# Performance work log

Hardware: AMD Instinct MI355X
Metric: run time of the kernel (lower is better)

The kernel has to match this reference:

```python
import jax, jax.numpy as jnp
import numpy as np

N = 50000
SELF_LOOP_W = 2.0  # GCNConv(improved=True)


def gcn_conv(x, edge_index, W, b):
    # x: [N, Fin], edge_index: [2, E] (row=source, col=target)
    h = x @ W  # [N, Fout]
    row, col = edge_index[0], edge_index[1]
    ones = jnp.ones(row.shape[0], dtype=h.dtype)
    deg = jax.ops.segment_sum(ones, col, num_segments=N) + SELF_LOOP_W
    dinv = jnp.where(deg > 0, jax.lax.rsqrt(deg), 0.0)
    norm = dinv[row] * dinv[col]  # [E]
    agg = jax.ops.segment_sum(norm[:, None] * h[row], col, num_segments=N)
    # self-loop contribution: weight 2.0, norm = dinv[i]^2
    agg = agg + (SELF_LOOP_W * dinv * dinv)[:, None] * h
    return agg + b


def setup_inputs() -> dict:
    key = jax.random.key(0)
    ks = jax.random.split(key, 12)
    F_in, H1, H2, H3 = 256, 256, 128, 64
    E, Ep, En = 800000, 200000, 200000
    def glorot(k, shape):
        lim = np.sqrt(6.0 / (shape[0] + shape[1]))
        return jax.random.uniform(k, shape, jnp.float32, -lim, lim)
    return {
        "x": jax.random.normal(ks[0], (N, F_in), jnp.float32),
        "train_edge_index": jax.random.randint(ks[1], (2, E), 0, N),
        "pos_edge_index": jax.random.randint(ks[2], (2, Ep), 0, N),
        "neg_edge_index": jax.random.randint(ks[3], (2, En), 0, N),
        "W1": glorot(ks[4], (F_in, H1)),
        "b1": jnp.zeros((H1,), jnp.float32),
        "W2": glorot(ks[5], (H1, H2)),
        "b2": jnp.zeros((H2,), jnp.float32),
        "Wl1": glorot(ks[6], (H2, H3)),
        "bl1": jnp.zeros((H3,), jnp.float32),
        "Wl2": glorot(ks[7], (H3, 1)),
        "bl2": jnp.zeros((1,), jnp.float32),
    }


def reference(x, train_edge_index, pos_edge_index, neg_edge_index,
              W1, b1, W2, b2, Wl1, bl1, Wl2, bl2):
    h = jax.nn.relu(gcn_conv(x, train_edge_index, W1, b1))
    h = gcn_conv(h, train_edge_index, W2, b2)  # [N, 128]
    tei = jnp.concatenate([pos_edge_index, neg_edge_index], axis=-1)  # [2, Ep+En]
    e = h[tei[1]] + h[tei[0]]  # x_i + x_j, [Etot, 128]
    e = jax.nn.relu(e @ Wl1 + bl1)
    e = jax.nn.sigmoid(e @ Wl2 + bl2)
    return e.reshape(-1)
```

## Files before the change

kernel.cpp:

```cpp
#include <hip/hip_runtime.h>
#include <math.h>

#define NV 50000
#define ETR 800000
#define EPOS 200000
#define ETEST 400000

typedef __attribute__((ext_vector_type(8))) short bf16x8;
typedef __attribute__((ext_vector_type(8))) unsigned short ushortx8;
typedef __attribute__((ext_vector_type(4))) float f32x4;

__device__ inline unsigned short f2b(float f) {
    union { float f; unsigned u; } v; v.f = f;
    unsigned r = v.u + 0x7fffu + ((v.u >> 16) & 1u);
    return (unsigned short)(r >> 16);
}
__device__ inline float blo(unsigned q) { union { unsigned u; float f; } v; v.u = q << 16; return v.f; }
__device__ inline float bhi(unsigned q) { union { unsigned u; float f; } v; v.u = q & 0xffff0000u; return v.f; }
__device__ inline float b2f(unsigned short s) { union { unsigned u; float f; } v; v.u = ((unsigned)s) << 16; return v.f; }

__device__ inline ushortx8 bf16add8(ushortx8 a, ushortx8 b) {
    ushortx8 r;
    #pragma unroll
    for (int i = 0; i < 8; ++i)
        r[i] = f2b(b2f(a[i]) + b2f(b[i]));
    return r;
}

#define GLOAD_LDS16(g, l) __builtin_amdgcn_global_load_lds( \
    (__attribute__((address_space(1))) void*)(g), \
    (__attribute__((address_space(3))) void*)(l), 16, 0, 0)


template<int N, int K, bool AF32>
__device__ __forceinline__ void gemm_body(
    const void* __restrict__ Av, const unsigned short* __restrict__ Bt,
    unsigned short* __restrict__ C, int M, int row0, int col0)
{
    constexpr int BK = 64;
    __shared__ unsigned short smem[18464];
    unsigned short (*Asm)[BK] = (unsigned short (*)[BK])smem;
    unsigned short (*Bsm)[BK] = (unsigned short (*)[BK])(smem + 8192);
    int tid = threadIdx.x;
    int lane = tid & 63, wid = tid >> 6;
    int wr = wid >> 1, wc = wid & 1;

    int sr = tid >> 3;
    int s8 = tid & 7;
    int fr = lane & 15;
    int g  = lane >> 4;

    f32x4 acc[4][4] = {};

    for (int k0 = 0; k0 < K; k0 += BK) {
        #pragma unroll
        for (int i = 0; i < 4; ++i) {
            int r = sr + i * 32;
            int gr = row0 + r;
            int s8sw = s8 ^ (r & 7);
            GLOAD_LDS16(&Bt[(size_t)(col0 + r) * K + k0 + s8sw * 8], &Bsm[r][s8 * 8]);
            if constexpr (AF32) {
                const float* Af = (const float*)Av;
                ushortx8 va = {0, 0, 0, 0, 0, 0, 0, 0};
                if (gr < M) {
                    float4 f0 = *(const float4*)&Af[(size_t)gr * K + k0 + s8 * 8];
                    float4 f1 = *(const float4*)&Af[(size_t)gr * K + k0 + s8 * 8 + 4];
                    va[0] = f2b(f0.x); va[1] = f2b(f0.y); va[2] = f2b(f0.z); va[3] = f2b(f0.w);
                    va[4] = f2b(f1.x); va[5] = f2b(f1.y); va[6] = f2b(f1.z); va[7] = f2b(f1.w);
                }
                *(ushortx8*)&Asm[r][(s8 ^ (r & 7)) * 8] = va;
            } else {
                const unsigned short* Ab = (const unsigned short*)Av;
                GLOAD_LDS16(&Ab[(size_t)gr * K + k0 + s8sw * 8], &Asm[r][s8 * 8]);
            }
        }
        __syncthreads();
        #pragma unroll
        for (int kf = 0; kf < BK; kf += 32) {
            int sbase = kf >> 3;
            bf16x8 af[4], bfr[4];
            #pragma unroll
            for (int m = 0; m < 4; ++m) {
                int rr = wr * 64 + m * 16 + fr;
                af[m] = *(const bf16x8*)&Asm[rr][((sbase + g) ^ (fr & 7)) * 8];
            }
            #pragma unroll
            for (int n = 0; n < 4; ++n) {
                int rr = wc * 64 + n * 16 + fr;
                bfr[n] = *(const bf16x8*)&Bsm[rr][((sbase + g) ^ (fr & 7)) * 8];
            }
            #pragma unroll
            for (int m = 0; m < 4; ++m)
                #pragma unroll
                for (int n = 0; n < 4; ++n)
                    acc[m][n] = __builtin_amdgcn_mfma_f32_16x16x32_bf16(af[m], bfr[n], acc[m][n], 0, 0, 0);
        }
        __syncthreads();
    }

    {
        unsigned short* cw = smem + wid * 4616;
        #pragma unroll
        for (int m = 0; m < 4; ++m)
            #pragma unroll
            for (int n = 0; n < 4; ++n)
                #pragma unroll
                for (int j = 0; j < 4; ++j)
                    cw[(m * 16 + g * 4 + j) * 72 + n * 16 + fr] = f2b(acc[m][n][j]);
        __syncthreads();
        int row = tid >> 1;
        int half = tid & 1;
        int q = ((row >> 6) << 1) + half;
        int rl = row & 63;
        const unsigned short* cr = smem + q * 4616 + rl * 72;
        int gr = row0 + row;
        if (gr < M) {
            unsigned short* gp = C + (size_t)gr * N + col0 + half * 64;
            #pragma unroll
            for (int c8 = 0; c8 < 8; ++c8)
                *(ushortx8*)&gp[c8 * 8] = *(const ushortx8*)&cr[c8 * 8];
        }
    }
}


__global__ __launch_bounds__(256) void fat0_kernel(
    const int* __restrict__ tei, int* __restrict__ deg,
    const float* __restrict__ W1, unsigned short* __restrict__ w1t)
{
    int bid = blockIdx.x;
    int t = threadIdx.x;
    if (bid < 3125) {
        int e = bid * 256 + t;
        if (e < ETR) atomicAdd(&deg[tei[ETR + e]], 1);
    } else {
        int i = (bid - 3125) * 256 + t;
        w1t[i] = f2b(W1[(i & 255) * 256 + (i >> 8)]);
    }
}


__global__ __launch_bounds__(1024) void ptr2_kernel(
    const int* __restrict__ deg, int* __restrict__ ptr,
    int* __restrict__ cursor, float* __restrict__ dinv)
{
    int b = blockIdx.x, t = threadIdx.x;
    int lane = t & 63, w = t >> 6;
    __shared__ int wred[16], wsum[16], woff[16];
    __shared__ int base_s;

    int pre = 0;
    int lim = b * 1024;
    for (int i = t; i < lim; i += 1024) pre += deg[i];
    #pragma unroll
    for (int off = 32; off > 0; off >>= 1) pre += __shfl_xor(pre, off);
    if (lane == 0) wred[w] = pre;
    __syncthreads();
    if (t == 0) {
        int s = 0;
        #pragma unroll
        for (int k = 0; k < 16; ++k) s += wred[k];
        base_s = s;
    }

    int i = b * 1024 + t;
    int d = (i < NV) ? deg[i] : 0;
    int v = d;
    #pragma unroll
    for (int off = 1; off < 64; off <<= 1) {
        int u = __shfl_up(v, off);
        if (lane >= off) v += u;
    }
    if (lane == 63) wsum[w] = v;
    __syncthreads();
    if (t == 0) {
        int s = base_s;
        #pragma unroll
        for (int k = 0; k < 16; ++k) { woff[k] = s; s += wsum[k]; }
    }
    __syncthreads();
    int excl = woff[w] + v - d;
    if (i < NV) {
        ptr[i] = excl;
        cursor[i] = excl;
        dinv[i] = rsqrtf((float)d + 2.0f);
        if (i == NV - 1) ptr[NV] = excl + d;
    }
}


__global__ __launch_bounds__(256) void fat1_kernel(
    const float* __restrict__ x, const unsigned short* __restrict__ w1t,
    unsigned short* __restrict__ h1lin,
    const int* __restrict__ tei, const float* __restrict__ dinv,
    int* __restrict__ cursor, int2* __restrict__ edat,
    const float* __restrict__ W2, unsigned short* __restrict__ w2t,
    const float* __restrict__ Wl1, unsigned short* __restrict__ wl1t)
{
    int bid = blockIdx.x;
    int t = threadIdx.x;
    if (bid < 782) {
        int row0 = (bid >> 1) * 128, col0 = (bid & 1) * 128;
        gemm_body<256, 256, true>(x, w1t, h1lin, NV, row0, col0);
    } else if (bid < 3907) {
        int e = (bid - 782) * 256 + t;
        if (e < ETR) {
            int row = tei[e];
            int col = tei[ETR + e];
            int p = atomicAdd(&cursor[col], 1);
            edat[p] = make_int2(row, __float_as_int(dinv[row] * dinv[col]));
        }
    } else if (bid < 4035) {
        int i = (bid - 3907) * 256 + t;
        w2t[i] = f2b(W2[(i & 255) * 128 + (i >> 8)]);
    } else {
        int i = (bid - 4035) * 256 + t;
        wl1t[i] = f2b(Wl1[(i & 127) * 64 + (i >> 7)]);
    }
}


__global__ __launch_bounds__(256) void gemm2_kernel(
    const unsigned short* __restrict__ A, const unsigned short* __restrict__ Bt,
    unsigned short* __restrict__ C)
{
    gemm_body<128, 256, false>(A, Bt, C, NV, blockIdx.x * 128, 0);
}


template<int F, bool RELU>
__global__ __launch_bounds__(256) void gather_kernel(
    const int* __restrict__ ptr, const int2* __restrict__ edat,
    const float* __restrict__ dinv, const unsigned short* __restrict__ hlin,
    const float* __restrict__ bias, unsigned short* __restrict__ hout)
{
    constexpr int V = F / 64;
    int gid = blockIdx.x * blockDim.x + threadIdx.x;
    int node = gid >> 6, lane = gid & 63;
    if (node >= NV) return;
    float dc = dinv[node];
    int j0 = ptr[node], j1 = ptr[node + 1];
    float acc[V] = {};
    const unsigned short* hb = hlin + lane * V;
    const long long* edl = (const long long*)edat;

    int j = j0;
    for (; j + 7 < j1; j += 8) {
        long long e[8];
        #pragma unroll
        for (int u = 0; u < 8; ++u) e[u] = __builtin_nontemporal_load(edl + j + u);
        if constexpr (V == 4) {
            uint2 q[8];
            #pragma unroll
            for (int u = 0; u < 8; ++u)
                q[u] = *(const uint2*)(hb + (size_t)(int)e[u] * F);
            #pragma unroll
            for (int u = 0; u < 8; ++u) {
                float n = __int_as_float((int)(e[u] >> 32));
                acc[0] += n * blo(q[u].x);
                acc[1] += n * bhi(q[u].x);
                acc[2] += n * blo(q[u].y);
                acc[3] += n * bhi(q[u].y);
            }
        } else {
            unsigned q[8];
            #pragma unroll
            for (int u = 0; u < 8; ++u)
                q[u] = *(const unsigned*)(hb + (size_t)(int)e[u] * F);
            #pragma unroll
            for (int u = 0; u < 8; ++u) {
                float n = __int_as_float((int)(e[u] >> 32));
                acc[0] += n * blo(q[u]);
                acc[1] += n * bhi(q[u]);
            }
        }
    }
    for (; j + 3 < j1; j += 4) {
        long long e[4];
        #pragma unroll
        for (int u = 0; u < 4; ++u) e[u] = __builtin_nontemporal_load(edl + j + u);
        if constexpr (V == 4) {
            uint2 q[4];
            #pragma unroll
            for (int u = 0; u < 4; ++u)
                q[u] = *(const uint2*)(hb + (size_t)(int)e[u] * F);
            #pragma unroll
            for (int u = 0; u < 4; ++u) {
                float n = __int_as_float((int)(e[u] >> 32));
                acc[0] += n * blo(q[u].x);
                acc[1] += n * bhi(q[u].x);
                acc[2] += n * blo(q[u].y);
                acc[3] += n * bhi(q[u].y);
            }
        } else {
            unsigned q[4];
            #pragma unroll
            for (int u = 0; u < 4; ++u)
                q[u] = *(const unsigned*)(hb + (size_t)(int)e[u] * F);
            #pragma unroll
            for (int u = 0; u < 4; ++u) {
                float n = __int_as_float((int)(e[u] >> 32));
                acc[0] += n * blo(q[u]);
                acc[1] += n * bhi(q[u]);
            }
        }
    }
    for (; j < j1; ++j) {
        long long e0 = __builtin_nontemporal_load(edl + j);
        float n0 = __int_as_float((int)(e0 >> 32));
        if constexpr (V == 4) {
            uint2 q0 = *(const uint2*)(hb + (size_t)(int)e0 * F);
            acc[0] += n0 * blo(q0.x);
            acc[1] += n0 * bhi(q0.x);
            acc[2] += n0 * blo(q0.y);
            acc[3] += n0 * bhi(q0.y);
        } else {
            unsigned q0 = *(const unsigned*)(hb + (size_t)(int)e0 * F);
            acc[0] += n0 * blo(q0);
            acc[1] += n0 * bhi(q0);
        }
    }

    const unsigned short* ps = hb + (size_t)node * F;
    float sw = 2.0f * dc * dc;
    if constexpr (V == 4) {
        uint2 qs = *(const uint2*)ps;
        float o0 = acc[0] + sw * blo(qs.x) + bias[lane * 4 + 0];
        float o1 = acc[1] + sw * bhi(qs.x) + bias[lane * 4 + 1];
        float o2 = acc[2] + sw * blo(qs.y) + bias[lane * 4 + 2];
        float o3 = acc[3] + sw * bhi(qs.y) + bias[lane * 4 + 3];
        if (RELU) {
            o0 = fmaxf(o0, 0.f); o1 = fmaxf(o1, 0.f);
            o2 = fmaxf(o2, 0.f); o3 = fmaxf(o3, 0.f);
        }
        union { unsigned short u[4]; unsigned long long ll; } pk;
        pk.u[0] = f2b(o0); pk.u[1] = f2b(o1); pk.u[2] = f2b(o2); pk.u[3] = f2b(o3);
        __builtin_nontemporal_store(pk.ll, (unsigned long long*)(hout + (size_t)node * F + lane * 4));
    } else {
        unsigned qs = *(const unsigned*)ps;
        float o0 = acc[0] + sw * blo(qs) + bias[lane * 2 + 0];
        float o1 = acc[1] + sw * bhi(qs) + bias[lane * 2 + 1];
        if (RELU) { o0 = fmaxf(o0, 0.f); o1 = fmaxf(o1, 0.f); }
        union { unsigned short u[2]; unsigned q; } pk;
        pk.u[0] = f2b(o0); pk.u[1] = f2b(o1);
        __builtin_nontemporal_store(pk.q, (unsigned*)(hout + (size_t)node * F + lane * 2));
    }
}


__global__ __launch_bounds__(256) void edge_mlp_mfma_kernel(
    const int* __restrict__ pos, const int* __restrict__ neg,
    const unsigned short* __restrict__ h2, const unsigned short* __restrict__ Wl1t,
    const float* __restrict__ bl1, const float* __restrict__ Wl2,
    const float* __restrict__ bl2, float* __restrict__ out)
{
    __shared__ unsigned short Es[128][128];
    __shared__ unsigned short Ws[64][128];
    int tid = threadIdx.x;
    int lane = tid & 63, w = tid >> 6;
    int fr = lane & 15, g = lane >> 4;
    int e0 = blockIdx.x * 128;

    #pragma unroll
    for (int k = 0; k < 4; ++k) {
        int chunk = tid + k * 256;
        int row = chunk >> 4, c = chunk & 15;
        *(ushortx8*)&Ws[row][(c ^ (row & 7)) * 8] = *(const ushortx8*)&Wl1t[chunk * 8];
    }

    int et = tid >> 1, hh = tid & 1;
    int eg = e0 + et;
    int a, b;
    if (eg < EPOS) { a = pos[eg]; b = pos[EPOS + eg]; }
    else { int i = eg - EPOS; a = neg[i]; b = neg[EPOS + i]; }
    const unsigned short* pa = h2 + (size_t)a * 128 + hh * 64;
    const unsigned short* pb = h2 + (size_t)b * 128 + hh * 64;
    #pragma unroll
    for (int c8 = 0; c8 < 8; ++c8) {
        ushortx8 va = *(const ushortx8*)&pa[c8 * 8];
        ushortx8 vb = *(const ushortx8*)&pb[c8 * 8];
        ushortx8 vs = bf16add8(va, vb);
        int c = hh * 8 + c8;
        *(ushortx8*)&Es[et][(c ^ (et & 7)) * 8] = vs;
    }
    __syncthreads();

    f32x4 acc[2][4] = {};
    #pragma unroll
    for (int ks = 0; ks < 4; ++ks) {
        int c = ks * 4 + g;
        bf16x8 af[2], bfr[4];
        #pragma unroll
        for (int m = 0; m < 2; ++m) {
            int r = w * 32 + m * 16 + fr;
            af[m] = *(const bf16x8*)&Es[r][(c ^ (r & 7)) * 8];
        }
        #pragma unroll
        for (int n = 0; n < 4; ++n) {
            int r = n * 16 + fr;
            bfr[n] = *(const bf16x8*)&Ws[r][(c ^ (r & 7)) * 8];
        }
        #pragma unroll
        for (int m = 0; m < 2; ++m)
            #pragma unroll
            for (int n = 0; n < 4; ++n)
                acc[m][n] = __builtin_amdgcn_mfma_f32_16x16x32_bf16(af[m], bfr[n], acc[m][n], 0, 0, 0);
    }

    float bl2v = bl2[0];
    float b1v[4], w2v[4];
    #pragma unroll
    for (int n = 0; n < 4; ++n) {
        b1v[n] = bl1[n * 16 + fr];
        w2v[n] = Wl2[n * 16 + fr];
    }
    #pragma unroll
    for (int m = 0; m < 2; ++m) {
        float p[4];
        #pragma unroll
        for (int j = 0; j < 4; ++j) {
            float s = 0.f;
            #pragma unroll
            for (int n = 0; n < 4; ++n)
                s += fmaxf(acc[m][n][j] + b1v[n], 0.0f) * w2v[n];
            p[j] = s;
        }
        #pragma unroll
        for (int off = 1; off < 16; off <<= 1) {
            #pragma unroll
            for (int j = 0; j < 4; ++j)
                p[j] += __shfl_xor(p[j], off);
        }
        int ebase = e0 + w * 32 + m * 16 + g * 4;
        #pragma unroll
        for (int j = 0; j < 4; ++j)
            if (fr == j)
                out[ebase + j] = 1.0f / (1.0f + expf(-(p[j] + bl2v)));
    }
}


extern "C" void kernel_launch(void* const* d_in, const int* in_sizes, int n_in,
                              void* d_out, int out_size, void* d_ws, size_t ws_size,
                              hipStream_t stream) {
    const float* x   = (const float*)d_in[0];
    const int*   tei = (const int*)d_in[1];
    const int*   pos = (const int*)d_in[2];
    const int*   neg = (const int*)d_in[3];
    const float* W1  = (const float*)d_in[4];
    const float* b1  = (const float*)d_in[5];
    const float* W2  = (const float*)d_in[6];
    const float* b2  = (const float*)d_in[7];
    const float* Wl1 = (const float*)d_in[8];
    const float* bl1 = (const float*)d_in[9];
    const float* Wl2 = (const float*)d_in[10];
    const float* bl2 = (const float*)d_in[11];
    float* out = (float*)d_out;

    float* fws = (float*)d_ws;
    int*   iws = (int*)d_ws;
    unsigned short* usws = (unsigned short*)d_ws;
    float* dinv     = fws;
    int*   deg      = iws + 50000;
    int*   ptr      = iws + 100000;
    int*   cursor   = iws + 150002;
    int2*  edat     = (int2*)(iws + 200064);
    unsigned short* w1t  = usws + 2ull * 1800192;
    unsigned short* w2t  = usws + 2ull * 1832960;
    unsigned short* wl1t = usws + 2ull * 1849344;
    unsigned short* bufX = usws + 2ull * 1853504;
    unsigned short* bufL16 = usws + 2ull * 8253504;
    unsigned short* bufH = usws + 2ull * 14653504;

    hipMemsetAsync(deg, 0, NV * sizeof(int), stream);

    fat0_kernel<<<3381, 256, 0, stream>>>(tei, deg, W1, w1t);

    ptr2_kernel<<<49, 1024, 0, stream>>>(deg, ptr, cursor, dinv);

    fat1_kernel<<<4067, 256, 0, stream>>>(x, w1t, bufL16, tei, dinv, cursor, edat,
                                          W2, w2t, Wl1, wl1t);

    gather_kernel<256, true><<<(NV * 64) / 256, 256, 0, stream>>>(ptr, edat, dinv, bufL16, b1, bufH);

    gemm2_kernel<<<391, 256, 0, stream>>>(bufH, w2t, bufX);
    gather_kernel<128, false><<<(NV * 64) / 256, 256, 0, stream>>>(ptr, edat, dinv, bufX, b2, bufL16);

    edge_mlp_mfma_kernel<<<ETEST / 128, 256, 0, stream>>>(pos, neg, bufL16, wl1t, bl1, Wl2, bl2, out);
}
```

Before: 281.3 us.

## Precompute per-node Wl1 projection then gather-add in edge head

Uses linearity: (h[a]+h[b])@Wl1 = h[a]@Wl1 + h[b]@Wl1, so a node-level GEMM (50k x 128 -> 64, padded to 128 columns with zeroed weights) computes u once, and the edge kernel gathers two 64-wide bf16 rows, adds bias, applies ReLU, dots with Wl2 and applies the sigmoid. This replaces 400k edge-level 128x64 MFMA work and 128-wide gathers with 64-wide gathers plus a smaller node GEMM. The cost is an extra kernel launch, a padded GEMM that wastes half its columns, and bf16 rounding of u before the add, which changes numerics slightly.

```diff
diff --git a/kernel.cpp b/kernel.cpp
--- a/kernel.cpp
+++ b/kernel.cpp
@@ -19,20 +19,12 @@
 __device__ inline float bhi(unsigned q) { union { unsigned u; float f; } v; v.u = q & 0xffff0000u; return v.f; }
 __device__ inline float b2f(unsigned short s) { union { unsigned u; float f; } v; v.u = ((unsigned)s) << 16; return v.f; }
 
-__device__ inline ushortx8 bf16add8(ushortx8 a, ushortx8 b) {
-    ushortx8 r;
-    #pragma unroll
-    for (int i = 0; i < 8; ++i)
-        r[i] = f2b(b2f(a[i]) + b2f(b[i]));
-    return r;
-}
-
 #define GLOAD_LDS16(g, l) __builtin_amdgcn_global_load_lds( \
     (__attribute__((address_space(1))) void*)(g), \
     (__attribute__((address_space(3))) void*)(l), 16, 0, 0)
 
 
-template<int N, int K, bool AF32>
+template<int N, int K, bool AF32, int NCOLS = N>
 __device__ __forceinline__ void gemm_body(
     const void* __restrict__ Av, const unsigned short* __restrict__ Bt,
     unsigned short* __restrict__ C, int M, int row0, int col0)
@@ -114,8 +106,8 @@
         int rl = row & 63;
         const unsigned short* cr = smem + q * 4616 + rl * 72;
         int gr = row0 + row;
-        if (gr < M) {
-            unsigned short* gp = C + (size_t)gr * N + col0 + half * 64;
+        if (gr < M && half * 64 < NCOLS) {
+            unsigned short* gp = C + (size_t)gr * NCOLS + col0 + half * 64;
             #pragma unroll
             for (int c8 = 0; c8 < 8; ++c8)
                 *(ushortx8*)&gp[c8 * 8] = *(const ushortx8*)&cr[c8 * 8];
@@ -213,9 +205,12 @@
     } else if (bid < 4035) {
         int i = (bid - 3907) * 256 + t;
         w2t[i] = f2b(W2[(i & 255) * 128 + (i >> 8)]);
-    } else {
+    } else if (bid < 4067) {
         int i = (bid - 4035) * 256 + t;
         wl1t[i] = f2b(Wl1[(i & 127) * 64 + (i >> 7)]);
+    } else {
+        int i = (bid - 4067) * 256 + t;
+        wl1t[8192 + i] = 0;
     }
 }
 
@@ -225,6 +220,13 @@
     unsigned short* __restrict__ C)
 {
     gemm_body<128, 256, false>(A, Bt, C, NV, blockIdx.x * 128, 0);
+}
+
+__global__ __launch_bounds__(256) void gemm_u_kernel(
+    const unsigned short* __restrict__ A, const unsigned short* __restrict__ Bt,
+    unsigned short* __restrict__ C)
+{
+    gemm_body<128, 128, false, 64>(A, Bt, C, NV, blockIdx.x * 128, 0);
 }
 
 
@@ -348,95 +350,33 @@
 }
 
 
-__global__ __launch_bounds__(256) void edge_mlp_mfma_kernel(
+__global__ __launch_bounds__(256) void edge_head_kernel(
     const int* __restrict__ pos, const int* __restrict__ neg,
-    const unsigned short* __restrict__ h2, const unsigned short* __restrict__ Wl1t,
+    const unsigned short* __restrict__ u,
     const float* __restrict__ bl1, const float* __restrict__ Wl2,
     const float* __restrict__ bl2, float* __restrict__ out)
 {
-    __shared__ unsigned short Es[128][128];
-    __shared__ unsigned short Ws[64][128];
     int tid = threadIdx.x;
-    int lane = tid & 63, w = tid >> 6;
-    int fr = lane & 15, g = lane >> 4;
-    int e0 = blockIdx.x * 128;
-
+    int wv = tid >> 6, lane = tid & 63;
+    int sub = lane >> 4, fl = lane & 15;
+    int e = blockIdx.x * 16 + wv * 4 + sub;
+    if (e >= ETEST) return;
+    int a, b;
+    if (e < EPOS) { a = pos[e]; b = pos[EPOS + e]; }
+    else { int i = e - EPOS; a = neg[i]; b = neg[EPOS + i]; }
+    uint2 qa = *(const uint2*)&u[(size_t)a * 64 + fl * 4];
+    uint2 qb = *(const uint2*)&u[(size_t)b * 64 + fl * 4];
+    float4 b1 = *(const float4*)&bl1[fl * 4];
+    float4 w2 = *(const float4*)&Wl2[fl * 4];
+    float s = fmaxf(blo(qa.x) + blo(qb.x) + b1.x, 0.f) * w2.x
+            + fmaxf(bhi(qa.x) + bhi(qb.x) + b1.y, 0.f) * w2.y
+            + fmaxf(blo(qa.y) + blo(qb.y) + b1.z, 0.f) * w2.z
+            + fmaxf(bhi(qa.y) + bhi(qb.y) + b1.w, 0.f) * w2.w;
     #pragma unroll
-    for (int k = 0; k < 4; ++k) {
-        int chunk = tid + k * 256;
-        int row = chunk >> 4, c = chunk & 15;
-        *(ushortx8*)&Ws[row][(c ^ (row & 7)) * 8] = *(const ushortx8*)&Wl1t[chunk * 8];
-    }
-
-    int et = tid >> 1, hh = tid & 1;
-    int eg = e0 + et;
-    int a, b;
-    if (eg < EPOS) { a = pos[eg]; b = pos[EPOS + eg]; }
-    else { int i = eg - EPOS; a = neg[i]; b = neg[EPOS + i]; }
-    const unsigned short* pa = h2 + (size_t)a * 128 + hh * 64;
-    const unsigned short* pb = h2 + (size_t)b * 128 + hh * 64;
-    #pragma unroll
-    for (int c8 = 0; c8 < 8; ++c8) {
-        ushortx8 va = *(const ushortx8*)&pa[c8 * 8];
-        ushortx8 vb = *(const ushortx8*)&pb[c8 * 8];
-        ushortx8 vs = bf16add8(va, vb);
-        int c = hh * 8 + c8;
-        *(ushortx8*)&Es[et][(c ^ (et & 7)) * 8] = vs;
-    }
-    __syncthreads();
-
-    f32x4 acc[2][4] = {};
-    #pragma unroll
-    for (int ks = 0; ks < 4; ++ks) {
-        int c = ks * 4 + g;
-        bf16x8 af[2], bfr[4];
-        #pragma unroll
-        for (int m = 0; m < 2; ++m) {
-            int r = w * 32 + m * 16 + fr;
-            af[m] = *(const bf16x8*)&Es[r][(c ^ (r & 7)) * 8];
-        }
-        #pragma unroll
-        for (int n = 0; n < 4; ++n) {
-            int r = n * 16 + fr;
-            bfr[n] = *(const bf16x8*)&Ws[r][(c ^ (r & 7)) * 8];
-        }
-        #pragma unroll
-        for (int m = 0; m < 2; ++m)
-            #pragma unroll
-            for (int n = 0; n < 4; ++n)
-                acc[m][n] = __builtin_amdgcn_mfma_f32_16x16x32_bf16(af[m], bfr[n], acc[m][n], 0, 0, 0);
-    }
-
-    float bl2v = bl2[0];
-    float b1v[4], w2v[4];
-    #pragma unroll
-    for (int n = 0; n < 4; ++n) {
-        b1v[n] = bl1[n * 16 + fr];
-        w2v[n] = Wl2[n * 16 + fr];
-    }
-    #pragma unroll
-    for (int m = 0; m < 2; ++m) {
-        float p[4];
-        #pragma unroll
-        for (int j = 0; j < 4; ++j) {
-            float s = 0.f;
-            #pragma unroll
-            for (int n = 0; n < 4; ++n)
-                s += fmaxf(acc[m][n][j] + b1v[n], 0.0f) * w2v[n];
-            p[j] = s;
-        }
-        #pragma unroll
-        for (int off = 1; off < 16; off <<= 1) {
-            #pragma unroll
-            for (int j = 0; j < 4; ++j)
-                p[j] += __shfl_xor(p[j], off);
-        }
-        int ebase = e0 + w * 32 + m * 16 + g * 4;
-        #pragma unroll
-        for (int j = 0; j < 4; ++j)
-            if (fr == j)
-                out[ebase + j] = 1.0f / (1.0f + expf(-(p[j] + bl2v)));
-    }
+    for (int off = 8; off > 0; off >>= 1)
+        s += __shfl_xor(s, off);
+    if (fl == 0)
+        out[e] = 1.0f / (1.0f + expf(-(s + bl2[0])));
 }
 
 
@@ -467,10 +407,11 @@
     int2*  edat     = (int2*)(iws + 200064);
     unsigned short* w1t  = usws + 2ull * 1800192;
     unsigned short* w2t  = usws + 2ull * 1832960;
-    unsigned short* wl1t = usws + 2ull * 1849344;
     unsigned short* bufX = usws + 2ull * 1853504;
     unsigned short* bufL16 = usws + 2ull * 8253504;
     unsigned short* bufH = usws + 2ull * 14653504;
+    unsigned short* wl1t = usws + 2ull * 21053504;
+    unsigned short* ubuf = usws + 2ull * 21061696;
 
     hipMemsetAsync(deg, 0, NV * sizeof(int), stream);
 
@@ -478,7 +419,7 @@
 
     ptr2_kernel<<<49, 1024, 0, stream>>>(deg, ptr, cursor, dinv);
 
-    fat1_kernel<<<4067, 256, 0, stream>>>(x, w1t, bufL16, tei, dinv, cursor, edat,
+    fat1_kernel<<<4099, 256, 0, stream>>>(x, w1t, bufL16, tei, dinv, cursor, edat,
                                           W2, w2t, Wl1, wl1t);
 
     gather_kernel<256, true><<<(NV * 64) / 256, 256, 0, stream>>>(ptr, edat, dinv, bufL16, b1, bufH);
@@ -486,5 +427,6 @@
     gemm2_kernel<<<391, 256, 0, stream>>>(bufH, w2t, bufX);
     gather_kernel<128, false><<<(NV * 64) / 256, 256, 0, stream>>>(ptr, edat, dinv, bufX, b2, bufL16);
 
-    edge_mlp_mfma_kernel<<<ETEST / 128, 256, 0, stream>>>(pos, neg, bufL16, wl1t, bl1, Wl2, bl2, out);
-}
+    gemm_u_kernel<<<391, 256, 0, stream>>>(bufL16, wl1t, ubuf);
+    edge_head_kernel<<<ETEST / 16, 256, 0, stream>>>(pos, neg, ubuf, bl1, Wl2, bl2, out);
+}
```

Result: faster. 262.8 us (-6.6%).
